# Kernel optimization log

Hardware: AMD Instinct MI355X
Metric: run time of the kernel (lower is better)

Reference implementation:

```python
import jax, jax.numpy as jnp
import numpy as np

RO = 4.0
STRIDE = 1.0
DILATIONS = (1, 1, 1, 2, 2, 4, 4)  # deep-snake res blocks


def conv2d(x, w, b, pad):
    y = jax.lax.conv_general_dilated(x, w, (1, 1), [(pad, pad), (pad, pad)],
                                     dimension_numbers=('NCHW', 'OIHW', 'NCHW'))
    return y + b[None, :, None, None]


def circ_conv(x, w, b, dilation):
    # x: [N, C, V]; circular (wrap) padding of n_adj*dilation on each side, kernel size 9 (n_adj=4)
    pad = (w.shape[-1] // 2) * dilation
    xp = jnp.concatenate([x[..., -pad:], x, x[..., :pad]], axis=-1)
    y = jax.lax.conv_general_dilated(xp, w, (1,), 'VALID', rhs_dilation=(dilation,),
                                     dimension_numbers=('NCH', 'OIH', 'NCH'))
    return y + b[None, :, None]


def bn(x, gamma, beta):
    # BatchNorm1d in eval mode (running_mean=0, running_var=1)
    return x * gamma[None, :, None] + beta[None, :, None]


def conv1x1(x, w, b):
    return jnp.einsum('oc,ncv->nov', w, x) + b[None, :, None]


def grid_sample_polys(feat, polys, ind):
    # feat: [B, C, H, W]; polys: [N, V, 2] (x, y) in feature-map pixel coords; ind: [N]
    # torch grid_sample(bilinear, align_corners=False, zeros pad) after the deep-snake
    # normalization x/(w/2)-1 reduces to sampling at (px-0.5, py-0.5).
    B, C, H, W = feat.shape
    ix = polys[..., 0] - 0.5
    iy = polys[..., 1] - 0.5
    x0 = jnp.floor(ix)
    y0 = jnp.floor(iy)
    wx = (ix - x0)[..., None]
    wy = (iy - y0)[..., None]
    x0i = x0.astype(jnp.int32)
    y0i = y0.astype(jnp.int32)

    def gather(yi, xi):
        valid = (xi >= 0) & (xi < W) & (yi >= 0) & (yi < H)
        xc = jnp.clip(xi, 0, W - 1)
        yc = jnp.clip(yi, 0, H - 1)
        v = feat[ind[:, None], :, yc, xc]  # [N, V, C]
        return v * valid[..., None]

    v00 = gather(y0i, x0i)
    v01 = gather(y0i, x0i + 1)
    v10 = gather(y0i + 1, x0i)
    v11 = gather(y0i + 1, x0i + 1)
    out = (v00 * (1 - wx) * (1 - wy) + v01 * wx * (1 - wy)
           + v10 * (1 - wx) * wy + v11 * wx * wy)
    return out.transpose(0, 2, 1)  # [N, C, V]


def snake_forward(x, head_w, head_b, head_g, head_bt, res_w, res_b, res_g, res_bt,
                  fus_w, fus_b, pw1, pb1, pw2, pb2, pw3, pb3):
    # Deep-snake Snake with conv_type='dgrid': head + 7 residual dilated circular convs,
    # fusion 1x1 + global max pool, then 3-layer 1x1 prediction head -> 2 offsets.
    h = bn(jax.nn.relu(circ_conv(x, head_w, head_b, 1)), head_g, head_bt)
    states = [h]
    cur = h
    for i, d in enumerate(DILATIONS):
        y = bn(jax.nn.relu(circ_conv(cur, res_w[i], res_b[i], d)), res_g[i], res_bt[i])
        cur = y + cur
        states.append(cur)
    state = jnp.concatenate(states, axis=1)  # [N, 8*state_dim, V]
    g = conv1x1(state, fus_w, fus_b)
    g = jnp.max(g, axis=2, keepdims=True)
    g = jnp.broadcast_to(g, (state.shape[0], g.shape[1], state.shape[2]))
    s = jnp.concatenate([g, state], axis=1)
    h1 = jax.nn.relu(conv1x1(s, pw1, pb1))
    h2 = jax.nn.relu(conv1x1(h1, pw2, pb2))
    return conv1x1(h2, pw3, pb3)  # [N, 2, V]


def setup_inputs() -> dict:
    key = jax.random.key(0)
    ks = jax.random.split(key, 24)
    B, C_IN, H, W = 8, 66, 128, 128
    NP, V = 128, 128
    SD = 128           # Snake state_dim = num_vertex
    FD = 66            # snake feature_dim = c_out_proj + 2
    K = 9              # 2*n_adj + 1
    nres = len(DILATIONS)
    s = 0.01  # torch init: normal_(0, 0.01)
    inp = {
        'cnn_feature': jax.random.normal(ks[0], (B, C_IN, H, W), jnp.float32),
        'i_it_poly': jax.random.uniform(ks[1], (NP, V, 2), jnp.float32) * (W - 1),
        'c_it_poly': jax.random.normal(ks[2], (NP, V, 2), jnp.float32) * 0.25,
        'ind': jax.random.randint(ks[3], (NP,), 0, B, jnp.int32),
        'proj_w1': jax.random.normal(ks[4], (256, C_IN, 3, 3), jnp.float32) * s,
        'proj_b1': jnp.zeros((256,), jnp.float32),
        'proj_w2': jax.random.normal(ks[5], (64, 256, 1, 1), jnp.float32) * s,
        'proj_b2': jnp.zeros((64,), jnp.float32),
        'head_w': jax.random.normal(ks[6], (SD, FD, K), jnp.float32) * s,
        'head_b': jnp.zeros((SD,), jnp.float32),
        'head_g': jnp.ones((SD,), jnp.float32),
        'head_bt': jnp.zeros((SD,), jnp.float32),
        'res_w': jax.random.normal(ks[7], (nres, SD, SD, K), jnp.float32) * s,
        'res_b': jnp.zeros((nres, SD), jnp.float32),
        'res_g': jnp.ones((nres, SD), jnp.float32),
        'res_bt': jnp.zeros((nres, SD), jnp.float32),
        'fus_w': jax.random.normal(ks[8], (256, SD * (nres + 1)), jnp.float32) * s,
        'fus_b': jnp.zeros((256,), jnp.float32),
        'pw1': jax.random.normal(ks[9], (256, SD * (nres + 1) + 256), jnp.float32) * s,
        'pb1': jnp.zeros((256,), jnp.float32),
        'pw2': jax.random.normal(ks[10], (64, 256), jnp.float32) * s,
        'pb2': jnp.zeros((64,), jnp.float32),
        'pw3': jax.random.normal(ks[11], (2, 64), jnp.float32) * s,
        'pb3': jnp.zeros((2,), jnp.float32),
    }
    return inp


def reference(cnn_feature, i_it_poly, c_it_poly, ind,
              proj_w1, proj_b1, proj_w2, proj_b2,
              head_w, head_b, head_g, head_bt,
              res_w, res_b, res_g, res_bt,
              fus_w, fus_b, pw1, pb1, pw2, pb2, pw3, pb3):
    # projection: conv3x3 -> relu -> conv1x1  (66 -> 256 -> 64)
    feat = jax.nn.relu(conv2d(cnn_feature, proj_w1, proj_b1, 1))
    feat = conv2d(feat, proj_w2, proj_b2, 0)
    # gather per-vertex features via bilinear grid sampling (get_gcn_feature)
    vert_feat = grid_sample_polys(feat, i_it_poly, ind)          # [N, 64, V]
    coords = (c_it_poly * RO).transpose(0, 2, 1)                  # [N, 2, V]
    init_input = jnp.concatenate([vert_feat, coords], axis=1)     # [N, 66, V]
    offset = snake_forward(init_input, head_w, head_b, head_g, head_bt,
                           res_w, res_b, res_g, res_bt,
                           fus_w, fus_b, pw1, pb1, pw2, pb2, pw3, pb3)
    i_poly = i_it_poly * RO + offset.transpose(0, 2, 1) * STRIDE  # [N, V, 2]
    return i_poly
```

## Files before the change

### kernel.cpp

```cpp
#include <hip/hip_runtime.h>
#include <hip/hip_bf16.h>

constexpr int B   = 8;
constexpr int CIN = 66;
constexpr int H   = 128, W = 128;
constexpr int C1  = 256;
constexpr int NP  = 128;
constexpr int V   = 128;
constexpr int SD  = 128;
constexpr int NRES = 7;
constexpr float RO = 4.0f;

typedef __bf16 bf16x8 __attribute__((ext_vector_type(8)));
typedef float  f32x4  __attribute__((ext_vector_type(4)));
typedef unsigned short u16x8 __attribute__((ext_vector_type(8)));

__device__ inline float bfu2f(unsigned short u) {
    union { unsigned int i; float f; } c; c.i = ((unsigned)u) << 16; return c.f;
}

__global__ __launch_bounds__(256) void k_pack_x(const float* __restrict__ x,
                                                __hip_bfloat16* __restrict__ xp)
{
    const int bi  = blockIdx.x;
    const int b   = bi / 130;
    const int yp  = bi % 130;
    const int tid = threadIdx.x;
    const int y   = yp - 1;
    const bool interior = (y >= 0 && y < H);

    __shared__ float xs[CIN * W];
    if (interior) {
        for (int i = tid; i < CIN * W; i += 256)
            xs[i] = x[((size_t)b * CIN + (i >> 7)) * (H * W) + y * W + (i & 127)];
    }
    __syncthreads();
    __hip_bfloat16* op = xp + ((size_t)b * 130 + yp) * (130 * 72);
    for (int i = tid; i < 130 * 72; i += 256) {
        int xpx = i / 72, c = i - xpx * 72;
        int xx = xpx - 1;
        float v = 0.f;
        if (interior && xx >= 0 && xx < W && c < CIN) v = xs[c * W + xx];
        op[i] = __float2bfloat16(v);
    }
}

__global__ __launch_bounds__(256) void k_pack_w(const float* __restrict__ w,
                                                __hip_bfloat16* __restrict__ wp)
{
    const int oc  = blockIdx.x;
    const int tid = threadIdx.x;
    for (int t = tid; t < 3 * 232; t += 256) {
        int ky = t / 232, s = t - ky * 232;
        float v = 0.f;
        if (s < 216) {
            int kx = s / 72, ic = s - kx * 72;
            if (ic < CIN) v = w[((size_t)(oc * CIN + ic) * 3 + ky) * 3 + kx];
        }
        wp[((size_t)ky * 256 + oc) * 232 + s] = __float2bfloat16(v);
    }
}

__global__ __launch_bounds__(256) void k_pack_snake_w(const float* __restrict__ hw,
                                                      const float* __restrict__ rw,
                                                      __hip_bfloat16* __restrict__ wpk2)
{
    const int l  = blockIdx.x >> 7;
    const int oc = blockIdx.x & 127;
    const int tid = threadIdx.x;
    for (int t = tid; t < 9 * 128; t += 256) {
        int k = t >> 7, ic = t & 127;
        float v = 0.f;
        if (l == 0) {
            if (ic < 66) v = hw[((size_t)oc * 66 + ic) * 9 + k];
        } else {
            v = rw[((((size_t)(l - 1) * 128 + oc) * 128) + ic) * 9 + k];
        }
        wpk2[(((size_t)l * 9 + k) * 128 + oc) * 128 + ic] = __float2bfloat16(v);
    }
}

__global__ __launch_bounds__(256) void k_pack_mat(const float* __restrict__ src,
                                                  __hip_bfloat16* __restrict__ dst,
                                                  int rows, int cols, int rstride, int coff)
{
    int n = rows * cols;
    for (int i = blockIdx.x * 256 + threadIdx.x; i < n; i += gridDim.x * 256) {
        int r = i / cols, c = i - r * cols;
        dst[i] = __float2bfloat16(src[(size_t)r * rstride + coff + c]);
    }
}

__global__ __launch_bounds__(256, 2) void k_conv3x3_mfma(
    const __hip_bfloat16* __restrict__ xp,
    const __hip_bfloat16* __restrict__ wp,
    const float* __restrict__ bias,
    __hip_bfloat16* __restrict__ out)
{
    __shared__ __hip_bfloat16 ash[3 * 9360 + 16];

    const int tid = threadIdx.x;
    const int ln  = tid & 63;
    const int wv  = tid >> 6;
    const int wm  = (wv >> 1) * 64;
    const int wn  = (wv & 1) * 64;
    const int l15 = ln & 15;
    const int lhi = ln >> 4;

    const int by  = blockIdx.x;
    const int b   = by >> 7;
    const int y   = by & 127;
    const int ocb = blockIdx.y * 128;

    {
        const char* g = (const char*)(xp + ((size_t)b * 130 + y) * 9360);
        for (int off = tid * 16; off < 56160; off += 4096)
            __builtin_amdgcn_global_load_lds(
                (const __attribute__((address_space(1))) void*)(g + off),
                (__attribute__((address_space(3))) void*)((char*)ash + off),
                16, 0, 0);
    }
    __syncthreads();

    f32x4 acc[4][4] = {};
#pragma unroll 1
    for (int ky = 0; ky < 3; ++ky) {
        const __hip_bfloat16* wk = wp + ((size_t)ky * 256 + ocb) * 232;
        const char* arow = (const char*)ash + ky * 18720;
#pragma unroll
        for (int ks = 0; ks < 7; ++ks) {
            bf16x8 a[4], bq[4];
#pragma unroll
            for (int m = 0; m < 4; ++m)
                a[m] = *(const bf16x8*)(arow + (wm + m * 16 + l15) * 144 + ks * 64 + lhi * 16);
#pragma unroll
            for (int n = 0; n < 4; ++n)
                bq[n] = *(const bf16x8*)(wk + (size_t)(wn + n * 16 + l15) * 232 + ks * 32 + lhi * 8);
#pragma unroll
            for (int m = 0; m < 4; ++m)
#pragma unroll
                for (int n = 0; n < 4; ++n)
                    acc[m][n] = __builtin_amdgcn_mfma_f32_16x16x32_bf16(
                        a[m], bq[n], acc[m][n], 0, 0, 0);
        }
    }

#pragma unroll
    for (int n = 0; n < 4; ++n) {
        int oc = ocb + wn + n * 16 + l15;
        float bb = bias[oc];
#pragma unroll
        for (int m = 0; m < 4; ++m) {
#pragma unroll
            for (int r = 0; r < 4; ++r) {
                int pos = wm + m * 16 + lhi * 4 + r;
                float v = acc[m][n][r] + bb;
                v = v > 0.f ? v : 0.f;
                out[(((size_t)b * 128 + y) * 128 + pos) * 256 + oc] = __float2bfloat16(v);
            }
        }
    }
}

__global__ __launch_bounds__(256) void k_conv1x1_mfma(
    const __hip_bfloat16* __restrict__ feat1,
    const __hip_bfloat16* __restrict__ w2b,
    const float* __restrict__ b2,
    __hip_bfloat16* __restrict__ feat2)
{
    const int tid = threadIdx.x;
    const int ln  = tid & 63;
    const int wv  = tid >> 6;
    const int wm  = wv * 64;
    const int l15 = ln & 15;
    const int lhi = ln >> 4;
    const int pos0 = blockIdx.x * 256;

    __shared__ __hip_bfloat16 wsh[64 * 136];
    for (int i = tid; i < 1024; i += 256) {
        int row = i >> 4, slot = i & 15;
        *(bf16x8*)&wsh[row * 136 + slot * 8] = *(const bf16x8*)(w2b + row * 256 + slot * 8);
    }
    __syncthreads();

    f32x4 acc[4][4] = {};
#pragma unroll
    for (int kk = 0; kk < 8; ++kk) {
        bf16x8 a[4], bq[4];
#pragma unroll
        for (int m = 0; m < 4; ++m)
            a[m] = *(const bf16x8*)(feat1 + (size_t)(pos0 + wm + m * 16 + l15) * 256 + kk * 32 + lhi * 8);
#pragma unroll
        for (int n = 0; n < 4; ++n)
            bq[n] = *(const bf16x8*)&wsh[(n * 16 + l15) * 136 + kk * 32 + lhi * 8];
#pragma unroll
        for (int m = 0; m < 4; ++m)
#pragma unroll
            for (int n = 0; n < 4; ++n)
                acc[m][n] = __builtin_amdgcn_mfma_f32_16x16x32_bf16(a[m], bq[n], acc[m][n], 0, 0, 0);
    }
#pragma unroll
    for (int n = 0; n < 4; ++n) {
        int og = n * 16 + l15;
        float bb = b2[og];
#pragma unroll
        for (int m = 0; m < 4; ++m)
#pragma unroll
            for (int r = 0; r < 4; ++r) {
                int pos = pos0 + wm + m * 16 + lhi * 4 + r;
                feat2[(size_t)pos * 64 + og] = __float2bfloat16(acc[m][n][r] + bb);
            }
    }
}

__global__ __launch_bounds__(256) void k_sample(
    const __hip_bfloat16* __restrict__ feat2, const float* __restrict__ ipoly,
    const float* __restrict__ cpoly, const int* __restrict__ ind,
    __hip_bfloat16* __restrict__ X0)
{
    const int p = blockIdx.x;
    const int v = threadIdx.x & 127;
    const int half = threadIdx.x >> 7;

    float px = ipoly[(p * V + v) * 2 + 0];
    float py = ipoly[(p * V + v) * 2 + 1];
    float ix = px - 0.5f, iy = py - 0.5f;
    float x0f = floorf(ix), y0f = floorf(iy);
    float wx = ix - x0f, wy = iy - y0f;
    int x0 = (int)x0f, y0 = (int)y0f;

    int   xsv[2] = {x0, x0 + 1}, ysv[2] = {y0, y0 + 1};
    float wxs[2] = {1.f - wx, wx}, wys[2] = {1.f - wy, wy};
    float cw[4]; int cbase[4];
#pragma unroll
    for (int jy = 0; jy < 2; ++jy)
#pragma unroll
        for (int jx = 0; jx < 2; ++jx) {
            int xi = xsv[jx], yi = ysv[jy];
            bool ok = (xi >= 0) && (xi < W) && (yi >= 0) && (yi < H);
            int xc = min(max(xi, 0), W - 1);
            int yc = min(max(yi, 0), H - 1);
            cw[jy * 2 + jx]    = wys[jy] * wxs[jx] * (ok ? 1.f : 0.f);
            cbase[jy * 2 + jx] = yc * W + xc;
        }

    const __hip_bfloat16* fb = feat2 + (size_t)ind[p] * (16384 * 64);
    __hip_bfloat16* xr = X0 + ((size_t)p * V + v) * 128;
#pragma unroll
    for (int ch = 0; ch < 4; ++ch) {
        int chh = half * 4 + ch;
        float s[8];
#pragma unroll
        for (int e = 0; e < 8; ++e) s[e] = 0.f;
#pragma unroll
        for (int j = 0; j < 4; ++j) {
            u16x8 t = *(const u16x8*)(fb + (size_t)cbase[j] * 64 + chh * 8);
#pragma unroll
            for (int e = 0; e < 8; ++e) s[e] += cw[j] * bfu2f(t[e]);
        }
#pragma unroll
        for (int e = 0; e < 8; ++e) xr[chh * 8 + e] = __float2bfloat16(s[e]);
    }
    if (half) {
        xr[64] = __float2bfloat16(cpoly[(p * V + v) * 2 + 0] * RO);
        xr[65] = __float2bfloat16(cpoly[(p * V + v) * 2 + 1] * RO);
        for (int c = 66; c < 128; ++c) xr[c] = __float2bfloat16(0.f);
    }
}

__global__ __launch_bounds__(256) void k_snake_mfma(
    const __hip_bfloat16* __restrict__ xin,
    const __hip_bfloat16* __restrict__ wl,
    const float* __restrict__ bias, const float* __restrict__ gamma,
    const float* __restrict__ beta,
    const __hip_bfloat16* __restrict__ resin,
    __hip_bfloat16* __restrict__ out,
    int dil)
{
    const int tid = threadIdx.x;
    const int ln  = tid & 63;
    const int wv  = tid >> 6;
    const int wm  = (wv >> 1) * 64;
    const int wn  = (wv & 1) * 32;
    const int l15 = ln & 15;
    const int lhi = ln >> 4;
    const int p   = blockIdx.x;
    const int ocb = blockIdx.y * 64;

    __shared__ __hip_bfloat16 xs[128 * 136];
    const __hip_bfloat16* xb = xin + (size_t)p * (V * 128);
    for (int i = tid; i < 2048; i += 256) {
        int v = i >> 4, slot = i & 15;
        *(bf16x8*)&xs[v * 136 + slot * 8] = *(const bf16x8*)(xb + v * 128 + slot * 8);
    }
    __syncthreads();

    f32x4 acc[4][2] = {};
#pragma unroll 1
    for (int k = 0; k < 9; ++k) {
        const int shift = (k - 4) * dil + 256;
        const __hip_bfloat16* wk = wl + (size_t)k * (128 * 128);
#pragma unroll
        for (int kc = 0; kc < 4; ++kc) {
            bf16x8 a[4], bq[2];
#pragma unroll
            for (int m = 0; m < 4; ++m) {
                int row = (wm + m * 16 + l15 + shift) & 127;
                a[m] = *(const bf16x8*)&xs[row * 136 + kc * 32 + lhi * 8];
            }
#pragma unroll
            for (int n = 0; n < 2; ++n)
                bq[n] = *(const bf16x8*)(wk + (size_t)(ocb + wn + n * 16 + l15) * 128 + kc * 32 + lhi * 8);
#pragma unroll
            for (int m = 0; m < 4; ++m)
#pragma unroll
                for (int n = 0; n < 2; ++n)
                    acc[m][n] = __builtin_amdgcn_mfma_f32_16x16x32_bf16(a[m], bq[n], acc[m][n], 0, 0, 0);
        }
    }

#pragma unroll
    for (int n = 0; n < 2; ++n) {
        int oc = ocb + wn + n * 16 + l15;
        float bb = bias[oc], gg = gamma[oc], bt = beta[oc];
#pragma unroll
        for (int m = 0; m < 4; ++m)
#pragma unroll
            for (int r = 0; r < 4; ++r) {
                int pos = wm + m * 16 + lhi * 4 + r;
                size_t idx = ((size_t)p * V + pos) * 128 + oc;
                float v = acc[m][n][r] + bb;
                v = v > 0.f ? v : 0.f;
                v = v * gg + bt;
                if (resin) v += __bfloat162float(resin[idx]);
                out[idx] = __float2bfloat16(v);
            }
    }
}

__global__ __launch_bounds__(256) void k_vconv1024(
    const __hip_bfloat16* __restrict__ xin,
    const __hip_bfloat16* __restrict__ wb,
    const float* __restrict__ fbias,
    const float* __restrict__ pbias,
    int relu,
    __hip_bfloat16* __restrict__ out)
{
    const int tid = threadIdx.x;
    const int ln  = tid & 63;
    const int wv  = tid >> 6;
    const int wm  = (wv >> 1) * 64;
    const int wn  = (wv & 1) * 64;
    const int l15 = ln & 15;
    const int lhi = ln >> 4;
    const int p   = blockIdx.x;
    const int ocb = blockIdx.y * 128;

    f32x4 acc[4][4] = {};
    for (int s = 0; s < 8; ++s) {
        const __hip_bfloat16* xa = xin + ((size_t)s * NP + p) * (V * 128);
#pragma unroll
        for (int kc = 0; kc < 4; ++kc) {
            bf16x8 a[4], bq[4];
#pragma unroll
            for (int m = 0; m < 4; ++m)
                a[m] = *(const bf16x8*)(xa + (size_t)(wm + m * 16 + l15) * 128 + kc * 32 + lhi * 8);
#pragma unroll
            for (int n = 0; n < 4; ++n)
                bq[n] = *(const bf16x8*)(wb + (size_t)(ocb + wn + n * 16 + l15) * 1024 + s * 128 + kc * 32 + lhi * 8);
#pragma unroll
            for (int m = 0; m < 4; ++m)
#pragma unroll
                for (int n = 0; n < 4; ++n)
                    acc[m][n] = __builtin_amdgcn_mfma_f32_16x16x32_bf16(a[m], bq[n], acc[m][n], 0, 0, 0);
        }
    }
#pragma unroll
    for (int n = 0; n < 4; ++n) {
        int og = ocb + wn + n * 16 + l15;
        float bb = (fbias ? fbias[og] : 0.f) + (pbias ? pbias[(size_t)p * 256 + og] : 0.f);
#pragma unroll
        for (int m = 0; m < 4; ++m)
#pragma unroll
            for (int r = 0; r < 4; ++r) {
                int pos = wm + m * 16 + lhi * 4 + r;
                float v = acc[m][n][r] + bb;
                if (relu) v = v > 0.f ? v : 0.f;
                out[((size_t)p * V + pos) * 256 + og] = __float2bfloat16(v);
            }
    }
}

__global__ __launch_bounds__(128) void k_h2(
    const __hip_bfloat16* __restrict__ h1,
    const __hip_bfloat16* __restrict__ w2b,
    const float* __restrict__ pb2,
    __hip_bfloat16* __restrict__ h2)
{
    const int tid = threadIdx.x;
    const int ln  = tid & 63;
    const int wv  = tid >> 6;
    const int wm  = wv * 64;
    const int l15 = ln & 15;
    const int lhi = ln >> 4;
    const int p   = blockIdx.x;

    f32x4 acc[4][4] = {};
#pragma unroll
    for (int kk = 0; kk < 8; ++kk) {
        bf16x8 a[4], bq[4];
#pragma unroll
        for (int m = 0; m < 4; ++m)
            a[m] = *(const bf16x8*)(h1 + ((size_t)p * V + wm + m * 16 + l15) * 256 + kk * 32 + lhi * 8);
#pragma unroll
        for (int n = 0; n < 4; ++n)
            bq[n] = *(const bf16x8*)(w2b + (size_t)(n * 16 + l15) * 256 + kk * 32 + lhi * 8);
#pragma unroll
        for (int m = 0; m < 4; ++m)
#pragma unroll
            for (int n = 0; n < 4; ++n)
                acc[m][n] = __builtin_amdgcn_mfma_f32_16x16x32_bf16(a[m], bq[n], acc[m][n], 0, 0, 0);
    }
#pragma unroll
    for (int n = 0; n < 4; ++n) {
        int og = n * 16 + l15;
        float bb = pb2[og];
#pragma unroll
        for (int m = 0; m < 4; ++m)
#pragma unroll
            for (int r = 0; r < 4; ++r) {
                int pos = wm + m * 16 + lhi * 4 + r;
                float v = acc[m][n][r] + bb;
                v = v > 0.f ? v : 0.f;
                h2[((size_t)p * V + pos) * 64 + og] = __float2bfloat16(v);
            }
    }
}

__global__ __launch_bounds__(256) void k_gmax(const __hip_bfloat16* __restrict__ fused,
                                              float* __restrict__ g)
{
    int p = blockIdx.x, o = threadIdx.x;
    float m = -3.4e38f;
    for (int v = 0; v < V; ++v)
        m = fmaxf(m, __bfloat162float(fused[((size_t)p * V + v) * 256 + o]));
    g[(size_t)p * 256 + o] = m;
}

__global__ __launch_bounds__(256) void k_gc(const float* __restrict__ g,
                                            const float* __restrict__ pw1,
                                            const float* __restrict__ pb1,
                                            float* __restrict__ gc)
{
    int p = blockIdx.x, o = threadIdx.x;
    __shared__ float gl[256];
    gl[o] = g[(size_t)p * 256 + o];
    __syncthreads();
    float a = pb1[o];
    const float* wr = pw1 + (size_t)o * 1280;
    for (int c = 0; c < 256; ++c) a += wr[c] * gl[c];
    gc[(size_t)p * 256 + o] = a;
}

__global__ __launch_bounds__(128) void k_final(const __hip_bfloat16* __restrict__ h2,
                                               const float* __restrict__ pw3,
                                               const float* __restrict__ pb3,
                                               const float* __restrict__ ipoly,
                                               float* __restrict__ outp)
{
    int p = blockIdx.x, v = threadIdx.x;
    __shared__ float w3[128];
    w3[v] = pw3[v];
    __syncthreads();
    float a0 = pb3[0], a1 = pb3[1];
    const u16x8* hp = (const u16x8*)(h2 + ((size_t)p * V + v) * 64);
#pragma unroll
    for (int ch = 0; ch < 8; ++ch) {
        u16x8 t = hp[ch];
#pragma unroll
        for (int e = 0; e < 8; ++e) {
            int c = ch * 8 + e;
            float hv = bfu2f(t[e]);
            a0 += w3[c] * hv;
            a1 += w3[64 + c] * hv;
        }
    }
    int idx = (p * V + v) * 2;
    outp[idx]     = ipoly[idx] * RO + a0;
    outp[idx + 1] = ipoly[idx + 1] * RO + a1;
}

extern "C" void kernel_launch(void* const* d_in, const int* in_sizes, int n_in,
                              void* d_out, int out_size, void* d_ws, size_t ws_size,
                              hipStream_t stream)
{
    const float* cnn   = (const float*)d_in[0];
    const float* ipoly = (const float*)d_in[1];
    const float* cpoly = (const float*)d_in[2];
    const int*   ind   = (const int*)d_in[3];
    const float* pw1c  = (const float*)d_in[4];
    const float* pb1c  = (const float*)d_in[5];
    const float* pw2c  = (const float*)d_in[6];
    const float* pb2c  = (const float*)d_in[7];
    const float* hw    = (const float*)d_in[8];
    const float* hb    = (const float*)d_in[9];
    const float* hg    = (const float*)d_in[10];
    const float* hbt   = (const float*)d_in[11];
    const float* rw    = (const float*)d_in[12];
    const float* rb    = (const float*)d_in[13];
    const float* rg    = (const float*)d_in[14];
    const float* rbt   = (const float*)d_in[15];
    const float* fw    = (const float*)d_in[16];
    const float* fb    = (const float*)d_in[17];
    const float* ppw1  = (const float*)d_in[18];
    const float* ppb1  = (const float*)d_in[19];
    const float* ppw2  = (const float*)d_in[20];
    const float* ppb2  = (const float*)d_in[21];
    const float* ppw3  = (const float*)d_in[22];
    const float* ppb3  = (const float*)d_in[23];
    float* outp = (float*)d_out;

    char* ws = (char*)d_ws;
    __hip_bfloat16* feat1  = (__hip_bfloat16*)(ws);
    __hip_bfloat16* states = (__hip_bfloat16*)(ws);
    __hip_bfloat16* fused  = (__hip_bfloat16*)(ws + 33554432);
    __hip_bfloat16* h1     = (__hip_bfloat16*)(ws + 41943040);
    __hip_bfloat16* h2     = (__hip_bfloat16*)(ws + 50331648);
    float*          gbuf   = (float*)(ws + 52428800);
    float*          gcbuf  = (float*)(ws + 52559872);
    __hip_bfloat16* xp     = (__hip_bfloat16*)(ws + 67108864);
    __hip_bfloat16* feat2  = (__hip_bfloat16*)(ws + 67108864);
    __hip_bfloat16* wpk    = (__hip_bfloat16*)(ws + 86577664);
    __hip_bfloat16* wpk2   = (__hip_bfloat16*)(ws + 87023104);
    __hip_bfloat16* fwb    = (__hip_bfloat16*)(ws + 89382400);
    __hip_bfloat16* pw1hb  = (__hip_bfloat16*)(ws + 89906688);
    __hip_bfloat16* pw2b   = (__hip_bfloat16*)(ws + 90430976);
    __hip_bfloat16* X0     = (__hip_bfloat16*)(ws + 90472448);

    k_pack_x<<<dim3(8 * 130), 256, 0, stream>>>(cnn, xp);
    k_pack_w<<<dim3(256), 256, 0, stream>>>(pw1c, wpk);
    k_pack_snake_w<<<dim3(8 * 128), 256, 0, stream>>>(hw, rw, wpk2);
    k_pack_mat<<<dim3(256), 256, 0, stream>>>(fw, fwb, 256, 1024, 1024, 0);
    k_pack_mat<<<dim3(256), 256, 0, stream>>>(ppw1, pw1hb, 256, 1024, 1280, 256);
    k_pack_mat<<<dim3(64), 256, 0, stream>>>(ppw2, pw2b, 64, 256, 256, 0);

    k_conv3x3_mfma<<<dim3(1024, 2), 256, 0, stream>>>(xp, wpk, pb1c, feat1);
    k_conv1x1_mfma<<<dim3(512), 256, 0, stream>>>(feat1, pw2b, pb2c, feat2);
    k_sample<<<dim3(NP), 256, 0, stream>>>(feat2, ipoly, cpoly, ind, X0);

    k_snake_mfma<<<dim3(NP, 2), 256, 0, stream>>>(X0, wpk2, hb, hg, hbt, nullptr,
                                                  states, 1);
    const int dil[NRES] = {1, 1, 1, 2, 2, 4, 4};
    const size_t SSZ = (size_t)NP * V * 128;
    for (int i = 0; i < NRES; ++i) {
        const __hip_bfloat16* xin = states + (size_t)i * SSZ;
        __hip_bfloat16* yout      = states + (size_t)(i + 1) * SSZ;
        const __hip_bfloat16* wi  = wpk2 + (size_t)(i + 1) * 9 * 128 * 128;
        k_snake_mfma<<<dim3(NP, 2), 256, 0, stream>>>(xin, wi, rb + i * SD, rg + i * SD,
                                                      rbt + i * SD, xin, yout, dil[i]);
    }

    k_vconv1024<<<dim3(NP, 2), 256, 0, stream>>>(states, fwb, fb, nullptr, 0, fused);
    k_gmax<<<dim3(NP), 256, 0, stream>>>(fused, gbuf);
    k_gc<<<dim3(NP), 256, 0, stream>>>(gbuf, ppw1, ppb1, gcbuf);
    k_vconv1024<<<dim3(NP, 2), 256, 0, stream>>>(states, pw1hb, nullptr, gcbuf, 1, h1);
    k_h2<<<dim3(NP), 128, 0, stream>>>(h1, pw2b, ppb2, h2);
    k_final<<<dim3(NP), 128, 0, stream>>>(h2, ppw3, ppb3, ipoly, outp);
}
```

Measured before the change: 497.2 us.

## Merge weight packing, stage conv3x3 weights in LDS, split snake grid, fuse gmax+gc

All five weight-packing kernels become one launch. The 3x3 conv now uses 64-output-channel tiles with a 4-wide grid and double-buffers its per-row weights into LDS through async global-to-LDS loads, instead of reading them from global memory. The snake kernel is split over position halves, using a 96-row halo window and a 4-wide grid for more blocks, and gmax and gc are fused into one kernel. Together these cut launch overhead and global weight reads and raise parallelism, at the cost of more LDS per block and redundant loading of the A tile in the conv.

```diff
diff --git a/kernel.cpp b/kernel.cpp
--- a/kernel.cpp
+++ b/kernel.cpp
@@ -45,108 +45,122 @@
     }
 }
 
-__global__ __launch_bounds__(256) void k_pack_w(const float* __restrict__ w,
-                                                __hip_bfloat16* __restrict__ wp)
-{
-    const int oc  = blockIdx.x;
-    const int tid = threadIdx.x;
-    for (int t = tid; t < 3 * 232; t += 256) {
-        int ky = t / 232, s = t - ky * 232;
-        float v = 0.f;
-        if (s < 216) {
-            int kx = s / 72, ic = s - kx * 72;
-            if (ic < CIN) v = w[((size_t)(oc * CIN + ic) * 3 + ky) * 3 + kx];
-        }
-        wp[((size_t)ky * 256 + oc) * 232 + s] = __float2bfloat16(v);
-    }
-}
-
-__global__ __launch_bounds__(256) void k_pack_snake_w(const float* __restrict__ hw,
-                                                      const float* __restrict__ rw,
-                                                      __hip_bfloat16* __restrict__ wpk2)
-{
-    const int l  = blockIdx.x >> 7;
-    const int oc = blockIdx.x & 127;
-    const int tid = threadIdx.x;
-    for (int t = tid; t < 9 * 128; t += 256) {
-        int k = t >> 7, ic = t & 127;
-        float v = 0.f;
-        if (l == 0) {
-            if (ic < 66) v = hw[((size_t)oc * 66 + ic) * 9 + k];
-        } else {
-            v = rw[((((size_t)(l - 1) * 128 + oc) * 128) + ic) * 9 + k];
-        }
-        wpk2[(((size_t)l * 9 + k) * 128 + oc) * 128 + ic] = __float2bfloat16(v);
-    }
-}
-
-__global__ __launch_bounds__(256) void k_pack_mat(const float* __restrict__ src,
-                                                  __hip_bfloat16* __restrict__ dst,
-                                                  int rows, int cols, int rstride, int coff)
-{
-    int n = rows * cols;
-    for (int i = blockIdx.x * 256 + threadIdx.x; i < n; i += gridDim.x * 256) {
-        int r = i / cols, c = i - r * cols;
-        dst[i] = __float2bfloat16(src[(size_t)r * rstride + coff + c]);
-    }
-}
-
-__global__ __launch_bounds__(256, 2) void k_conv3x3_mfma(
+__global__ __launch_bounds__(256) void k_pack_weights(
+    const float* __restrict__ w3, const float* __restrict__ hw,
+    const float* __restrict__ rw, const float* __restrict__ fw,
+    const float* __restrict__ ppw1, const float* __restrict__ ppw2,
+    __hip_bfloat16* __restrict__ wp2, __hip_bfloat16* __restrict__ wpk2,
+    __hip_bfloat16* __restrict__ fwb, __hip_bfloat16* __restrict__ pw1hb,
+    __hip_bfloat16* __restrict__ pw2b)
+{
+    const int bid = blockIdx.x, tid = threadIdx.x;
+    if (bid < 256) {
+        int oc = bid, ocg = bid >> 6, ocl = bid & 63;
+        for (int t = tid; t < 3 * 232; t += 256) {
+            int ky = t / 232, s = t - ky * 232;
+            float v = 0.f;
+            if (s < 216) {
+                int kx = s / 72, ic = s - kx * 72;
+                if (ic < CIN) v = w3[((size_t)(oc * CIN + ic) * 3 + ky) * 3 + kx];
+            }
+            wp2[(((size_t)ky * 4 + ocg) * 64 + ocl) * 232 + s] = __float2bfloat16(v);
+        }
+    } else if (bid < 1280) {
+        int q = bid - 256, l = q >> 7, oc = q & 127;
+        for (int t = tid; t < 9 * 128; t += 256) {
+            int k = t >> 7, ic = t & 127;
+            float v = 0.f;
+            if (l == 0) { if (ic < 66) v = hw[((size_t)oc * 66 + ic) * 9 + k]; }
+            else v = rw[((((size_t)(l - 1) * 128 + oc) * 128) + ic) * 9 + k];
+            wpk2[(((size_t)l * 9 + k) * 128 + oc) * 128 + ic] = __float2bfloat16(v);
+        }
+    } else if (bid < 1536) {
+        int r = bid - 1280;
+        for (int c = tid; c < 1024; c += 256)
+            fwb[(size_t)r * 1024 + c] = __float2bfloat16(fw[(size_t)r * 1024 + c]);
+    } else if (bid < 1792) {
+        int r = bid - 1536;
+        for (int c = tid; c < 1024; c += 256)
+            pw1hb[(size_t)r * 1024 + c] = __float2bfloat16(ppw1[(size_t)r * 1280 + 256 + c]);
+    } else {
+        int r = bid - 1792;
+        for (int c = tid; c < 256; c += 256)
+            pw2b[(size_t)r * 256 + c] = __float2bfloat16(ppw2[(size_t)r * 256 + c]);
+    }
+}
+
+__global__ __launch_bounds__(256) void k_conv3x3_mfma(
     const __hip_bfloat16* __restrict__ xp,
-    const __hip_bfloat16* __restrict__ wp,
+    const __hip_bfloat16* __restrict__ wp2,
     const float* __restrict__ bias,
     __hip_bfloat16* __restrict__ out)
 {
-    __shared__ __hip_bfloat16 ash[3 * 9360 + 16];
+    __shared__ __hip_bfloat16 ash[28112];
+    __shared__ __hip_bfloat16 bsh[2 * 14848];
 
     const int tid = threadIdx.x;
     const int ln  = tid & 63;
     const int wv  = tid >> 6;
     const int wm  = (wv >> 1) * 64;
-    const int wn  = (wv & 1) * 64;
+    const int wn  = (wv & 1) * 32;
     const int l15 = ln & 15;
     const int lhi = ln >> 4;
 
     const int by  = blockIdx.x;
     const int b   = by >> 7;
     const int y   = by & 127;
-    const int ocb = blockIdx.y * 128;
+    const int ocg = blockIdx.y;
+    const int ocb = ocg * 64;
 
     {
         const char* g = (const char*)(xp + ((size_t)b * 130 + y) * 9360);
         for (int off = tid * 16; off < 56160; off += 4096)
             __builtin_amdgcn_global_load_lds(
                 (const __attribute__((address_space(1))) void*)(g + off),
-                (__attribute__((address_space(3))) void*)((char*)ash + off),
-                16, 0, 0);
+                (__attribute__((address_space(3))) void*)((char*)ash + off), 16, 0, 0);
+        const char* gb = (const char*)(wp2 + ((size_t)0 * 4 + ocg) * 14848);
+        for (int off = tid * 16; off < 29696; off += 4096)
+            __builtin_amdgcn_global_load_lds(
+                (const __attribute__((address_space(1))) void*)(gb + off),
+                (__attribute__((address_space(3))) void*)((char*)bsh + off), 16, 0, 0);
+        if (tid < 32) ash[28080 + tid] = __float2bfloat16(0.f);
     }
     __syncthreads();
 
-    f32x4 acc[4][4] = {};
-#pragma unroll 1
+    f32x4 acc[4][2] = {};
+#pragma unroll
     for (int ky = 0; ky < 3; ++ky) {
-        const __hip_bfloat16* wk = wp + ((size_t)ky * 256 + ocb) * 232;
+        if (ky < 2) {
+            const char* gb = (const char*)(wp2 + ((size_t)(ky + 1) * 4 + ocg) * 14848);
+            char* dst = (char*)bsh + ((ky + 1) & 1) * 29696;
+            for (int off = tid * 16; off < 29696; off += 4096)
+                __builtin_amdgcn_global_load_lds(
+                    (const __attribute__((address_space(1))) void*)(gb + off),
+                    (__attribute__((address_space(3))) void*)(dst + off), 16, 0, 0);
+        }
         const char* arow = (const char*)ash + ky * 18720;
+        const char* bb   = (const char*)bsh + (ky & 1) * 29696;
 #pragma unroll
         for (int ks = 0; ks < 7; ++ks) {
-            bf16x8 a[4], bq[4];
+            bf16x8 a[4], bq[2];
 #pragma unroll
             for (int m = 0; m < 4; ++m)
                 a[m] = *(const bf16x8*)(arow + (wm + m * 16 + l15) * 144 + ks * 64 + lhi * 16);
 #pragma unroll
-            for (int n = 0; n < 4; ++n)
-                bq[n] = *(const bf16x8*)(wk + (size_t)(wn + n * 16 + l15) * 232 + ks * 32 + lhi * 8);
+            for (int n = 0; n < 2; ++n)
+                bq[n] = *(const bf16x8*)(bb + (wn + n * 16 + l15) * 464 + ks * 64 + lhi * 16);
 #pragma unroll
             for (int m = 0; m < 4; ++m)
 #pragma unroll
-                for (int n = 0; n < 4; ++n)
+                for (int n = 0; n < 2; ++n)
                     acc[m][n] = __builtin_amdgcn_mfma_f32_16x16x32_bf16(
                         a[m], bq[n], acc[m][n], 0, 0, 0);
         }
-    }
-
-#pragma unroll
-    for (int n = 0; n < 4; ++n) {
+        __syncthreads();
+    }
+
+#pragma unroll
+    for (int n = 0; n < 2; ++n) {
         int oc = ocb + wn + n * 16 + l15;
         float bb = bias[oc];
 #pragma unroll
@@ -280,39 +294,43 @@
     const int tid = threadIdx.x;
     const int ln  = tid & 63;
     const int wv  = tid >> 6;
-    const int wm  = (wv >> 1) * 64;
+    const int wm  = (wv >> 1) * 32;
     const int wn  = (wv & 1) * 32;
     const int l15 = ln & 15;
     const int lhi = ln >> 4;
     const int p   = blockIdx.x;
-    const int ocb = blockIdx.y * 64;
-
-    __shared__ __hip_bfloat16 xs[128 * 136];
+    const int mg  = blockIdx.y >> 1;
+    const int og  = blockIdx.y & 1;
+    const int pos0 = mg * 64;
+    const int ocb  = og * 64;
+
+    __shared__ __hip_bfloat16 xs[96 * 136];
     const __hip_bfloat16* xb = xin + (size_t)p * (V * 128);
-    for (int i = tid; i < 2048; i += 256) {
-        int v = i >> 4, slot = i & 15;
-        *(bf16x8*)&xs[v * 136 + slot * 8] = *(const bf16x8*)(xb + v * 128 + slot * 8);
+    for (int i = tid; i < 96 * 16; i += 256) {
+        int r = i >> 4, slot = i & 15;
+        int grow = (pos0 - 16 + r) & 127;
+        *(bf16x8*)&xs[r * 136 + slot * 8] = *(const bf16x8*)(xb + (size_t)grow * 128 + slot * 8);
     }
     __syncthreads();
 
-    f32x4 acc[4][2] = {};
+    f32x4 acc[2][2] = {};
 #pragma unroll 1
     for (int k = 0; k < 9; ++k) {
-        const int shift = (k - 4) * dil + 256;
+        const int ofs = (k - 4) * dil + 16;
         const __hip_bfloat16* wk = wl + (size_t)k * (128 * 128);
 #pragma unroll
         for (int kc = 0; kc < 4; ++kc) {
-            bf16x8 a[4], bq[2];
-#pragma unroll
-            for (int m = 0; m < 4; ++m) {
-                int row = (wm + m * 16 + l15 + shift) & 127;
+            bf16x8 a[2], bq[2];
+#pragma unroll
+            for (int m = 0; m < 2; ++m) {
+                int row = wm + m * 16 + l15 + ofs;
                 a[m] = *(const bf16x8*)&xs[row * 136 + kc * 32 + lhi * 8];
             }
 #pragma unroll
             for (int n = 0; n < 2; ++n)
                 bq[n] = *(const bf16x8*)(wk + (size_t)(ocb + wn + n * 16 + l15) * 128 + kc * 32 + lhi * 8);
 #pragma unroll
-            for (int m = 0; m < 4; ++m)
+            for (int m = 0; m < 2; ++m)
 #pragma unroll
                 for (int n = 0; n < 2; ++n)
                     acc[m][n] = __builtin_amdgcn_mfma_f32_16x16x32_bf16(a[m], bq[n], acc[m][n], 0, 0, 0);
@@ -324,10 +342,10 @@
         int oc = ocb + wn + n * 16 + l15;
         float bb = bias[oc], gg = gamma[oc], bt = beta[oc];
 #pragma unroll
-        for (int m = 0; m < 4; ++m)
+        for (int m = 0; m < 2; ++m)
 #pragma unroll
             for (int r = 0; r < 4; ++r) {
-                int pos = wm + m * 16 + lhi * 4 + r;
+                int pos = pos0 + wm + m * 16 + lhi * 4 + r;
                 size_t idx = ((size_t)p * V + pos) * 128 + oc;
                 float v = acc[m][n][r] + bb;
                 v = v > 0.f ? v : 0.f;
@@ -437,24 +455,17 @@
     }
 }
 
-__global__ __launch_bounds__(256) void k_gmax(const __hip_bfloat16* __restrict__ fused,
-                                              float* __restrict__ g)
+__global__ __launch_bounds__(256) void k_gmaxgc(const __hip_bfloat16* __restrict__ fused,
+                                                const float* __restrict__ pw1,
+                                                const float* __restrict__ pb1,
+                                                float* __restrict__ gc)
 {
     int p = blockIdx.x, o = threadIdx.x;
     float m = -3.4e38f;
     for (int v = 0; v < V; ++v)
         m = fmaxf(m, __bfloat162float(fused[((size_t)p * V + v) * 256 + o]));
-    g[(size_t)p * 256 + o] = m;
-}
-
-__global__ __launch_bounds__(256) void k_gc(const float* __restrict__ g,
-                                            const float* __restrict__ pw1,
-                                            const float* __restrict__ pb1,
-                                            float* __restrict__ gc)
-{
-    int p = blockIdx.x, o = threadIdx.x;
     __shared__ float gl[256];
-    gl[o] = g[(size_t)p * 256 + o];
+    gl[o] = m;
     __syncthreads();
     float a = pb1[o];
     const float* wr = pw1 + (size_t)o * 1280;
@@ -526,29 +537,25 @@
     __hip_bfloat16* fused  = (__hip_bfloat16*)(ws + 33554432);
     __hip_bfloat16* h1     = (__hip_bfloat16*)(ws + 41943040);
     __hip_bfloat16* h2     = (__hip_bfloat16*)(ws + 50331648);
-    float*          gbuf   = (float*)(ws + 52428800);
-    float*          gcbuf  = (float*)(ws + 52559872);
+    float*          gcbuf  = (float*)(ws + 52428800);
     __hip_bfloat16* xp     = (__hip_bfloat16*)(ws + 67108864);
     __hip_bfloat16* feat2  = (__hip_bfloat16*)(ws + 67108864);
-    __hip_bfloat16* wpk    = (__hip_bfloat16*)(ws + 86577664);
-    __hip_bfloat16* wpk2   = (__hip_bfloat16*)(ws + 87023104);
-    __hip_bfloat16* fwb    = (__hip_bfloat16*)(ws + 89382400);
-    __hip_bfloat16* pw1hb  = (__hip_bfloat16*)(ws + 89906688);
-    __hip_bfloat16* pw2b   = (__hip_bfloat16*)(ws + 90430976);
-    __hip_bfloat16* X0     = (__hip_bfloat16*)(ws + 90472448);
+    __hip_bfloat16* wp2    = (__hip_bfloat16*)(ws + 86577664);
+    __hip_bfloat16* wpk2   = (__hip_bfloat16*)(ws + 86934016);
+    __hip_bfloat16* fwb    = (__hip_bfloat16*)(ws + 89293312);
+    __hip_bfloat16* pw1hb  = (__hip_bfloat16*)(ws + 89817600);
+    __hip_bfloat16* pw2b   = (__hip_bfloat16*)(ws + 90341888);
+    __hip_bfloat16* X0     = (__hip_bfloat16*)(ws + 90374656);
 
     k_pack_x<<<dim3(8 * 130), 256, 0, stream>>>(cnn, xp);
-    k_pack_w<<<dim3(256), 256, 0, stream>>>(pw1c, wpk);
-    k_pack_snake_w<<<dim3(8 * 128), 256, 0, stream>>>(hw, rw, wpk2);
-    k_pack_mat<<<dim3(256), 256, 0, stream>>>(fw, fwb, 256, 1024, 1024, 0);
-    k_pack_mat<<<dim3(256), 256, 0, stream>>>(ppw1, pw1hb, 256, 1024, 1280, 256);
-    k_pack_mat<<<dim3(64), 256, 0, stream>>>(ppw2, pw2b, 64, 256, 256, 0);
-
-    k_conv3x3_mfma<<<dim3(1024, 2), 256, 0, stream>>>(xp, wpk, pb1c, feat1);
+    k_pack_weights<<<dim3(1856), 256, 0, stream>>>(pw1c, hw, rw, fw, ppw1, ppw2,
+                                                   wp2, wpk2, fwb, pw1hb, pw2b);
+
+    k_conv3x3_mfma<<<dim3(1024, 4), 256, 0, stream>>>(xp, wp2, pb1c, feat1);
     k_conv1x1_mfma<<<dim3(512), 256, 0, stream>>>(feat1, pw2b, pb2c, feat2);
     k_sample<<<dim3(NP), 256, 0, stream>>>(feat2, ipoly, cpoly, ind, X0);
 
-    k_snake_mfma<<<dim3(NP, 2), 256, 0, stream>>>(X0, wpk2, hb, hg, hbt, nullptr,
+    k_snake_mfma<<<dim3(NP, 4), 256, 0, stream>>>(X0, wpk2, hb, hg, hbt, nullptr,
                                                   states, 1);
     const int dil[NRES] = {1, 1, 1, 2, 2, 4, 4};
     const size_t SSZ = (size_t)NP * V * 128;
@@ -556,13 +563,12 @@
         const __hip_bfloat16* xin = states + (size_t)i * SSZ;
         __hip_bfloat16* yout      = states + (size_t)(i + 1) * SSZ;
         const __hip_bfloat16* wi  = wpk2 + (size_t)(i + 1) * 9 * 128 * 128;
-        k_snake_mfma<<<dim3(NP, 2), 256, 0, stream>>>(xin, wi, rb + i * SD, rg + i * SD,
+        k_snake_mfma<<<dim3(NP, 4), 256, 0, stream>>>(xin, wi, rb + i * SD, rg + i * SD,
                                                       rbt + i * SD, xin, yout, dil[i]);
     }
 
     k_vconv1024<<<dim3(NP, 2), 256, 0, stream>>>(states, fwb, fb, nullptr, 0, fused);
-    k_gmax<<<dim3(NP), 256, 0, stream>>>(fused, gbuf);
-    k_gc<<<dim3(NP), 256, 0, stream>>>(gbuf, ppw1, ppb1, gcbuf);
+    k_gmaxgc<<<dim3(NP), 256, 0, stream>>>(fused, ppw1, ppb1, gcbuf);
     k_vconv1024<<<dim3(NP, 2), 256, 0, stream>>>(states, pw1hb, nullptr, gcbuf, 1, h1);
     k_h2<<<dim3(NP), 128, 0, stream>>>(h1, pw2b, ppb2, h2);
     k_final<<<dim3(NP), 128, 0, stream>>>(h2, ppw3, ppb3, ipoly, outp);
```

New measurement: 556.7 us. +12.0%, slower.
